# Optimization experiments

Measured on AMD Instinct MI355X. Metric: run time of the kernel, lower is better.

Reference implementation:

```python
import jax, jax.numpy as jnp
import numpy as np

T, D, H, S = 32768, 512, 1024, 256  # seq_len, observation_dim, hidden_size, state_dim


def setup_inputs() -> dict:
    key = jax.random.key(0)
    ks = jax.random.split(key, 8)
    lim_ih = 1.0 / np.sqrt(H)
    return {
        "y": jax.random.normal(ks[0], (T, D), dtype=jnp.float32),
        "h0": jax.random.normal(ks[1], (H,), dtype=jnp.float32),
        "w_ih": jax.random.uniform(ks[2], (3 * H, D), minval=-lim_ih, maxval=lim_ih, dtype=jnp.float32),
        "w_hh": jax.random.uniform(ks[3], (3 * H, H), minval=-lim_ih, maxval=lim_ih, dtype=jnp.float32),
        "b": jax.random.uniform(ks[4], (3 * H,), minval=-lim_ih, maxval=lim_ih, dtype=jnp.float32),
        "bn": jax.random.uniform(ks[5], (H,), minval=-lim_ih, maxval=lim_ih, dtype=jnp.float32),
        "w_out": jax.random.uniform(ks[6], (2 * S, H), minval=-lim_ih, maxval=lim_ih, dtype=jnp.float32),
        "b_out": jax.random.uniform(ks[7], (2 * S,), minval=-lim_ih, maxval=lim_ih, dtype=jnp.float32),
    }


def _gru_forward(y, h0, w_ih, w_hh, b, bn):
    # Precompute input-side gates for all timesteps in one GEMM: [T, 3H]
    igates = y @ w_ih.T + b

    def step(h, ig):
        ir, iz, inn = jnp.split(ig, 3)
        hg = w_hh @ h  # [3H]
        hr, hz, hn = jnp.split(hg, 3)
        r = jax.nn.sigmoid(ir + hr)
        z = jax.nn.sigmoid(iz + hz)  # equinox calls this `inp`
        n = jnp.tanh(inn + r * (hn + bn))
        h_new = n + z * (h - n)
        return h_new, h_new

    _, hs = jax.lax.scan(step, jnp.tanh(h0), igates)
    return hs  # [T, H]


def reference(y, h0, w_ih, w_hh, b, bn, w_out, b_out):
    hs = _gru_forward(y, h0, w_ih, w_hh, b, bn)
    out = hs @ w_out.T + b_out  # [T, 2S]
    nat1, nat2 = jnp.split(out, 2, axis=-1)
    return (nat1, jax.nn.softplus(nat2))
```

## Files before the change

### kernel.cpp

```cpp
#include <hip/hip_runtime.h>
#include <math.h>

#define T_STEPS 32768
#define DIM 512
#define HID 1024
#define SD 256

#define NWG 256
#define RBT 128

typedef unsigned u32x4 __attribute__((ext_vector_type(4)));

#define PIN4(v) asm volatile("" : "+v"((v).x), "+v"((v).y), "+v"((v).z), "+v"((v).w))

__device__ __forceinline__ float dot4(float4 a, float4 b) {
    return a.x*b.x + a.y*b.y + a.z*b.z + a.w*b.w;
}
__device__ __forceinline__ float sigmoid_fast(float x) {
    float e = __builtin_amdgcn_exp2f(-1.4426950408889634f * x);
    return __builtin_amdgcn_rcpf(1.f + e);
}
__device__ __forceinline__ float tanh_fast(float x) {
    float e = __builtin_amdgcn_exp2f(2.8853900817779268f * x);
    return 1.f - 2.f * __builtin_amdgcn_rcpf(e + 1.f);
}
__device__ __forceinline__ float softplus_f(float x) {
    float ax = fabsf(x);
    return fmaxf(x, 0.f) + log1pf(expf(-ax));
}
__device__ __forceinline__ float4 asf4(u32x4 q) {
    return make_float4(__uint_as_float(q.x), __uint_as_float(q.y),
                       __uint_as_float(q.z), __uint_as_float(q.w));
}

__device__ __forceinline__ float wave_sum(float v) {
    int x;
    x = __builtin_amdgcn_mov_dpp(__float_as_int(v), 0xB1,  0xf, 0xf, true); v += __int_as_float(x);
    x = __builtin_amdgcn_mov_dpp(__float_as_int(v), 0x4E,  0xf, 0xf, true); v += __int_as_float(x);
    x = __builtin_amdgcn_mov_dpp(__float_as_int(v), 0x141, 0xf, 0xf, true); v += __int_as_float(x);
    x = __builtin_amdgcn_mov_dpp(__float_as_int(v), 0x128, 0xf, 0xf, true); v += __int_as_float(x);
    v += __shfl_xor(v, 16, 64);
    v += __shfl_xor(v, 32, 64);
    return v;
}

__global__ void init_kernel(const float* __restrict__ h0,
                            unsigned* __restrict__ htag) {
    int i = blockIdx.x * 256 + threadIdx.x;
    unsigned v = __float_as_uint(tanhf(h0[i]));
    htag[i]       = v & ~3u;
    htag[HID + i] = 0u;
}

#define TAGCHK(m, tg)                                                          \
    m = ((q0.x ^ tg) | (q0.y ^ tg)) | ((q0.z ^ tg) | (q0.w ^ tg))              \
      | ((q1.x ^ tg) | (q1.y ^ tg)) | ((q1.z ^ tg) | (q1.w ^ tg))              \
      | ((q2.x ^ tg) | (q2.y ^ tg)) | ((q2.z ^ tg) | (q2.w ^ tg))              \
      | ((q3.x ^ tg) | (q3.y ^ tg)) | ((q3.z ^ tg) | (q3.w ^ tg))

__global__ __launch_bounds__(RBT, 1) void gru_scan(
    const float* __restrict__ y, const float* __restrict__ h0,
    const float* __restrict__ w_ih, const float* __restrict__ w_hh,
    const float* __restrict__ b, const float* __restrict__ bn,
    const float* __restrict__ w_out, const float* __restrict__ b_out,
    float* __restrict__ out, unsigned* __restrict__ htag ) {
    const int tid  = threadIdx.x;
    const int wg   = blockIdx.x;
    const int wv   = tid >> 6;
    const int lane = tid & 63;
    const int half = lane >> 5;
    const int u0   = wg * 4 + wv * 2;
    const int um   = u0 + half;

    float4 wh[3][2][4];
    #pragma unroll
    for (int g = 0; g < 3; ++g)
        #pragma unroll
        for (int uu = 0; uu < 2; ++uu) {
            const float* row = &w_hh[(size_t)(g * HID + u0 + uu) * HID + 16 * lane];
            #pragma unroll
            for (int q = 0; q < 4; ++q) { wh[g][uu][q] = *(const float4*)&row[4*q]; PIN4(wh[g][uu][q]); }
        }
    float4 wi[3][2][2];
    #pragma unroll
    for (int g = 0; g < 3; ++g)
        #pragma unroll
        for (int uu = 0; uu < 2; ++uu) {
            const float* row = &w_ih[(size_t)(g * HID + u0 + uu) * DIM + 8 * lane];
            #pragma unroll
            for (int q = 0; q < 2; ++q) { wi[g][uu][q] = *(const float4*)&row[4*q]; PIN4(wi[g][uu][q]); }
        }
    const int c = 2 * wg + wv;
    float4 wo[4];
    #pragma unroll
    for (int q = 0; q < 4; ++q) {
        wo[q] = *(const float4*)&w_out[(size_t)c * HID + 16 * lane + 4 * q];
        PIN4(wo[q]);
    }

    const float bi_r = b[um], bi_z = b[HID + um], bi_n = b[2 * HID + um];
    const float bnu  = bn[um];
    const float bo   = b_out[c];

    float hp = tanhf(h0[um]);

    float yr, yz, yi;
    {
        float4 ya0 = *(const float4*)&y[8 * lane];
        float4 ya1 = *(const float4*)&y[8 * lane + 4];
        float d[6];
        #pragma unroll
        for (int g = 0; g < 3; ++g)
            #pragma unroll
            for (int uu = 0; uu < 2; ++uu)
                d[g*2+uu] = dot4(wi[g][uu][0], ya0) + dot4(wi[g][uu][1], ya1);
        #pragma unroll
        for (int k = 0; k < 6; ++k) d[k] = wave_sum(d[k]);
        yr = (half ? d[1] : d[0]) + bi_r;
        yz = (half ? d[3] : d[2]) + bi_z;
        yi = (half ? d[5] : d[4]) + bi_n;
    }

    const size_t TS = (size_t)T_STEPS * SD;

    for (int t = 0; t <= T_STEPS; ++t) {
        const unsigned tg = (unsigned)t & 3u;
        const unsigned* pa = htag + (size_t)((t & 1) * HID + 16 * lane);
        const int tn = (t + 1 < T_STEPS) ? (t + 1) : 0;
        const float* ya = &y[(size_t)tn * DIM + 8 * lane];

        u32x4 q0, q1, q2, q3, yq0, yq1;
        asm volatile(
            "global_load_dwordx4 %[y0], %[ya], off\n\t"
            "global_load_dwordx4 %[y1], %[ya], off offset:16\n\t"
            "global_load_dwordx4 %[q0], %[pa], off sc0 sc1\n\t"
            "global_load_dwordx4 %[q1], %[pa], off offset:16 sc0 sc1\n\t"
            "global_load_dwordx4 %[q2], %[pa], off offset:32 sc0 sc1\n\t"
            "global_load_dwordx4 %[q3], %[pa], off offset:48 sc0 sc1\n\t"
            "s_waitcnt vmcnt(0)"
            : [q0]"=&v"(q0), [q1]"=&v"(q1), [q2]"=&v"(q2), [q3]"=&v"(q3),
              [y0]"=&v"(yq0), [y1]"=&v"(yq1)
            : [pa]"v"(pa), [ya]"v"(ya)
            : "memory");
        unsigned m; TAGCHK(m, tg);
        while ((m & 3u) != 0u) {
            asm volatile(
                "global_load_dwordx4 %[q0], %[pa], off sc0 sc1\n\t"
                "global_load_dwordx4 %[q1], %[pa], off offset:16 sc0 sc1\n\t"
                "global_load_dwordx4 %[q2], %[pa], off offset:32 sc0 sc1\n\t"
                "global_load_dwordx4 %[q3], %[pa], off offset:48 sc0 sc1\n\t"
                "s_waitcnt vmcnt(0)"
                : [q0]"=&v"(q0), [q1]"=&v"(q1), [q2]"=&v"(q2), [q3]"=&v"(q3)
                : [pa]"v"(pa)
                : "memory");
            TAGCHK(m, tg);
        }
        float4 hv0 = asf4(q0), hv1 = asf4(q1), hv2 = asf4(q2), hv3 = asf4(q3);

        if (t < T_STEPS) {
            float s[6];
            #pragma unroll
            for (int g = 0; g < 3; ++g)
                #pragma unroll
                for (int uu = 0; uu < 2; ++uu)
                    s[g*2+uu] = dot4(wh[g][uu][0], hv0) + dot4(wh[g][uu][1], hv1)
                              + dot4(wh[g][uu][2], hv2) + dot4(wh[g][uu][3], hv3);
            #pragma unroll
            for (int k = 0; k < 6; ++k) s[k] = wave_sum(s[k]);

            float r = sigmoid_fast((half ? s[1] : s[0]) + yr);
            float z = sigmoid_fast((half ? s[3] : s[2]) + yz);
            float n = tanh_fast(yi + r * ((half ? s[5] : s[4]) + bnu));
            float hnew = n + z * (hp - n);
            hp = hnew;

            if ((lane & 31) == 0) {
                unsigned pv = (__float_as_uint(hnew) & ~3u) | (((unsigned)t + 1u) & 3u);
                unsigned* pp = htag + (size_t)(((t + 1) & 1) * HID + um);
                asm volatile("global_store_dword %0, %1, off sc0 sc1"
                             :: "v"(pp), "v"(pv) : "memory");
            }
            __builtin_amdgcn_sched_barrier(0);
        }

        {
            float4 ya0 = asf4(yq0), ya1 = asf4(yq1);
            float d[6];
            #pragma unroll
            for (int g = 0; g < 3; ++g)
                #pragma unroll
                for (int uu = 0; uu < 2; ++uu)
                    d[g*2+uu] = dot4(wi[g][uu][0], ya0) + dot4(wi[g][uu][1], ya1);
            #pragma unroll
            for (int k = 0; k < 6; ++k) d[k] = wave_sum(d[k]);
            yr = (half ? d[1] : d[0]) + bi_r;
            yz = (half ? d[3] : d[2]) + bi_z;
            yi = (half ? d[5] : d[4]) + bi_n;
        }

        if (t > 0) {
            float p = dot4(wo[0], hv0) + dot4(wo[1], hv1)
                    + dot4(wo[2], hv2) + dot4(wo[3], hv3);
            p = wave_sum(p);
            if (lane == 0) {
                float v = p + bo;
                size_t row = (size_t)(t - 1);
                if (c >= SD) out[TS + row * SD + (c - SD)] = softplus_f(v);
                else         out[row * SD + c] = v;
            }
        }
    }
}

extern "C" void kernel_launch(void* const* d_in, const int* in_sizes, int n_in,
                              void* d_out, int out_size, void* d_ws, size_t ws_size,
                              hipStream_t stream) {
    const float* y     = (const float*)d_in[0];
    const float* h0    = (const float*)d_in[1];
    const float* w_ih  = (const float*)d_in[2];
    const float* w_hh  = (const float*)d_in[3];
    const float* b     = (const float*)d_in[4];
    const float* bn    = (const float*)d_in[5];
    const float* w_out = (const float*)d_in[6];
    const float* b_out = (const float*)d_in[7];
    float* out = (float*)d_out;

    unsigned* htag = (unsigned*)d_ws;

    hipLaunchKernelGGL(init_kernel, dim3(4), dim3(256), 0, stream, h0, htag);
    hipLaunchKernelGGL(gru_scan, dim3(NWG), dim3(RBT), 0, stream,
                       y, h0, w_ih, w_hh, b, bn, w_out, b_out, out, htag);
}
```

Before: 52.11 ms.

## Split GRU scan into recurrent and helper waves communicating through LDS

Doubles the workgroup to four waves: two waves handle only the recurrent w_hh matvec and global h exchange, while two helper waves compute the input projection for future timesteps and the output projection plus softplus. They hand off data through shared-memory ring buffers guarded by volatile sequence counters. The aim is to take the input-GEMV and output work off the serial critical path of each timestep. The cost is extra LDS traffic, intra-workgroup spin-waiting, and the risk that the helper waves fall behind and stall the recurrence.

```diff
diff --git a/kernel.cpp b/kernel.cpp
--- a/kernel.cpp
+++ b/kernel.cpp
@@ -7,7 +7,7 @@
 #define SD 256
 
 #define NWG 256
-#define RBT 128
+#define RBT 256
 
 typedef unsigned u32x4 __attribute__((ext_vector_type(4)));
 
@@ -52,11 +52,24 @@
     htag[HID + i] = 0u;
 }
 
-#define TAGCHK(m, tg)                                                          \
-    m = ((q0.x ^ tg) | (q0.y ^ tg)) | ((q0.z ^ tg) | (q0.w ^ tg))              \
-      | ((q1.x ^ tg) | (q1.y ^ tg)) | ((q1.z ^ tg) | (q1.w ^ tg))              \
-      | ((q2.x ^ tg) | (q2.y ^ tg)) | ((q2.z ^ tg) | (q2.w ^ tg))              \
-      | ((q3.x ^ tg) | (q3.y ^ tg)) | ((q3.z ^ tg) | (q3.w ^ tg))
+__device__ __forceinline__ void spin1(const unsigned* pa, unsigned tg,
+                                      u32x4& q0, u32x4& q1, u32x4& q2, u32x4& q3) {
+    for (;;) {
+        asm volatile(
+            "global_load_dwordx4 %0, %4, off sc0 sc1\n\t"
+            "global_load_dwordx4 %1, %4, off offset:16 sc0 sc1\n\t"
+            "global_load_dwordx4 %2, %4, off offset:32 sc0 sc1\n\t"
+            "global_load_dwordx4 %3, %4, off offset:48 sc0 sc1\n\t"
+            "s_waitcnt vmcnt(0)"
+            : "=&v"(q0), "=&v"(q1), "=&v"(q2), "=&v"(q3)
+            : "v"(pa) : "memory");
+        unsigned m = ((q0.x ^ tg) | (q0.y ^ tg)) | ((q0.z ^ tg) | (q0.w ^ tg))
+                   | ((q1.x ^ tg) | (q1.y ^ tg)) | ((q1.z ^ tg) | (q1.w ^ tg))
+                   | ((q2.x ^ tg) | (q2.y ^ tg)) | ((q2.z ^ tg) | (q2.w ^ tg))
+                   | ((q3.x ^ tg) | (q3.y ^ tg)) | ((q3.z ^ tg) | (q3.w ^ tg));
+        if ((m & 3u) == 0u) break;
+    }
+}
 
 __global__ __launch_bounds__(RBT, 1) void gru_scan(
     const float* __restrict__ y, const float* __restrict__ h0,
@@ -69,122 +82,120 @@
     const int wv   = tid >> 6;
     const int lane = tid & 63;
     const int half = lane >> 5;
-    const int u0   = wg * 4 + wv * 2;
-    const int um   = u0 + half;
-
-    float4 wh[3][2][4];
-    #pragma unroll
-    for (int g = 0; g < 3; ++g)
-        #pragma unroll
-        for (int uu = 0; uu < 2; ++uu) {
-            const float* row = &w_hh[(size_t)(g * HID + u0 + uu) * HID + 16 * lane];
-            #pragma unroll
-            for (int q = 0; q < 4; ++q) { wh[g][uu][q] = *(const float4*)&row[4*q]; PIN4(wh[g][uu][q]); }
+
+    __shared__ float hsh[2][HID];
+    __shared__ float ygv[4][2][6];
+    __shared__ int   seqH[2];
+    __shared__ int   seqY[8];
+    __shared__ int   prog[2];
+    if (tid < 2) { seqH[tid] = 0; prog[tid] = 0; }
+    if (tid < 8) seqY[tid] = 0;
+    __syncthreads();
+    volatile int* vseqH = seqH;
+    volatile int* vseqY = seqY;
+    volatile int* vprog = prog;
+
+    const size_t TS = (size_t)T_STEPS * SD;
+
+    if (wv < 2) {
+        const int u0 = wg * 4 + wv * 2;
+        const int um = u0 + half;
+
+        float4 wh[3][2][4];
+        #pragma unroll
+        for (int g = 0; g < 3; ++g)
+            #pragma unroll
+            for (int uu = 0; uu < 2; ++uu) {
+                const float* row = &w_hh[(size_t)(g * HID + u0 + uu) * HID + 16 * lane];
+                #pragma unroll
+                for (int q = 0; q < 4; ++q) { wh[g][uu][q] = *(const float4*)&row[4*q]; PIN4(wh[g][uu][q]); }
+            }
+        const float bnu = bn[um];
+        float hp = tanhf(h0[um]);
+
+        for (int t = 0; t <= T_STEPS; ++t) {
+            const unsigned tg = (unsigned)t & 3u;
+            const unsigned* pa = htag + (size_t)((t & 1) * HID + 16 * lane);
+            u32x4 q0, q1, q2, q3;
+            spin1(pa, tg, q0, q1, q2, q3);
+            float4 hv0 = asf4(q0), hv1 = asf4(q1), hv2 = asf4(q2), hv3 = asf4(q3);
+
+            if (t < T_STEPS) {
+                volatile int* sy = &vseqY[(t & 3) * 2 + wv];
+                while (*sy != t + 1) {}
+                asm volatile("" ::: "memory");
+                const float* yB = ygv[t & 3][wv];
+                float yr = yB[half * 3 + 0];
+                float yz = yB[half * 3 + 1];
+                float yi = yB[half * 3 + 2];
+
+                float s[6];
+                #pragma unroll
+                for (int g = 0; g < 3; ++g)
+                    #pragma unroll
+                    for (int uu = 0; uu < 2; ++uu)
+                        s[g*2+uu] = dot4(wh[g][uu][0], hv0) + dot4(wh[g][uu][1], hv1)
+                                  + dot4(wh[g][uu][2], hv2) + dot4(wh[g][uu][3], hv3);
+                #pragma unroll
+                for (int k = 0; k < 6; ++k) s[k] = wave_sum(s[k]);
+
+                float r = sigmoid_fast((half ? s[1] : s[0]) + yr);
+                float z = sigmoid_fast((half ? s[3] : s[2]) + yz);
+                float n = tanh_fast(yi + r * ((half ? s[5] : s[4]) + bnu));
+                float hnew = n + z * (hp - n);
+                hp = hnew;
+
+                if ((lane & 31) == 0) {
+                    unsigned pv = (__float_as_uint(hnew) & ~3u) | (((unsigned)t + 1u) & 3u);
+                    unsigned* pp = htag + (size_t)(((t + 1) & 1) * HID + um);
+                    asm volatile("global_store_dword %0, %1, off sc0 sc1"
+                                 :: "v"(pp), "v"(pv) : "memory");
+                }
+                __builtin_amdgcn_sched_barrier(0);
+            }
+
+            if (wv == 0) {
+                while (vprog[0] < t - 1 || vprog[1] < t - 1) {}
+                asm volatile("" ::: "memory");
+                float* hd = &hsh[t & 1][16 * lane];
+                *(float4*)&hd[0]  = hv0;
+                *(float4*)&hd[4]  = hv1;
+                *(float4*)&hd[8]  = hv2;
+                *(float4*)&hd[12] = hv3;
+                asm volatile("s_waitcnt lgkmcnt(0)" ::: "memory");
+                if (lane == 0) vseqH[t & 1] = t + 1;
+            }
         }
-    float4 wi[3][2][2];
-    #pragma unroll
-    for (int g = 0; g < 3; ++g)
-        #pragma unroll
-        for (int uu = 0; uu < 2; ++uu) {
-            const float* row = &w_ih[(size_t)(g * HID + u0 + uu) * DIM + 8 * lane];
-            #pragma unroll
-            for (int q = 0; q < 2; ++q) { wi[g][uu][q] = *(const float4*)&row[4*q]; PIN4(wi[g][uu][q]); }
+    } else {
+        const int hw  = wv - 2;
+        const int us0 = wg * 4 + hw * 2;
+
+        float4 wi[3][2][2];
+        #pragma unroll
+        for (int g = 0; g < 3; ++g)
+            #pragma unroll
+            for (int uu = 0; uu < 2; ++uu) {
+                const float* row = &w_ih[(size_t)(g * HID + us0 + uu) * DIM + 8 * lane];
+                #pragma unroll
+                for (int q = 0; q < 2; ++q) { wi[g][uu][q] = *(const float4*)&row[4*q]; PIN4(wi[g][uu][q]); }
+            }
+        const int c = 2 * wg + hw;
+        float4 wo[4];
+        #pragma unroll
+        for (int q = 0; q < 4; ++q) {
+            wo[q] = *(const float4*)&w_out[(size_t)c * HID + 16 * lane + 4 * q];
+            PIN4(wo[q]);
         }
-    const int c = 2 * wg + wv;
-    float4 wo[4];
-    #pragma unroll
-    for (int q = 0; q < 4; ++q) {
-        wo[q] = *(const float4*)&w_out[(size_t)c * HID + 16 * lane + 4 * q];
-        PIN4(wo[q]);
-    }
-
-    const float bi_r = b[um], bi_z = b[HID + um], bi_n = b[2 * HID + um];
-    const float bnu  = bn[um];
-    const float bo   = b_out[c];
-
-    float hp = tanhf(h0[um]);
-
-    float yr, yz, yi;
-    {
-        float4 ya0 = *(const float4*)&y[8 * lane];
-        float4 ya1 = *(const float4*)&y[8 * lane + 4];
-        float d[6];
+        const float bo = b_out[c];
+        float bb[6];
         #pragma unroll
         for (int g = 0; g < 3; ++g)
             #pragma unroll
-            for (int uu = 0; uu < 2; ++uu)
-                d[g*2+uu] = dot4(wi[g][uu][0], ya0) + dot4(wi[g][uu][1], ya1);
-        #pragma unroll
-        for (int k = 0; k < 6; ++k) d[k] = wave_sum(d[k]);
-        yr = (half ? d[1] : d[0]) + bi_r;
-        yz = (half ? d[3] : d[2]) + bi_z;
-        yi = (half ? d[5] : d[4]) + bi_n;
-    }
-
-    const size_t TS = (size_t)T_STEPS * SD;
-
-    for (int t = 0; t <= T_STEPS; ++t) {
-        const unsigned tg = (unsigned)t & 3u;
-        const unsigned* pa = htag + (size_t)((t & 1) * HID + 16 * lane);
-        const int tn = (t + 1 < T_STEPS) ? (t + 1) : 0;
-        const float* ya = &y[(size_t)tn * DIM + 8 * lane];
-
-        u32x4 q0, q1, q2, q3, yq0, yq1;
-        asm volatile(
-            "global_load_dwordx4 %[y0], %[ya], off\n\t"
-            "global_load_dwordx4 %[y1], %[ya], off offset:16\n\t"
-            "global_load_dwordx4 %[q0], %[pa], off sc0 sc1\n\t"
-            "global_load_dwordx4 %[q1], %[pa], off offset:16 sc0 sc1\n\t"
-            "global_load_dwordx4 %[q2], %[pa], off offset:32 sc0 sc1\n\t"
-            "global_load_dwordx4 %[q3], %[pa], off offset:48 sc0 sc1\n\t"
-            "s_waitcnt vmcnt(0)"
-            : [q0]"=&v"(q0), [q1]"=&v"(q1), [q2]"=&v"(q2), [q3]"=&v"(q3),
-              [y0]"=&v"(yq0), [y1]"=&v"(yq1)
-            : [pa]"v"(pa), [ya]"v"(ya)
-            : "memory");
-        unsigned m; TAGCHK(m, tg);
-        while ((m & 3u) != 0u) {
-            asm volatile(
-                "global_load_dwordx4 %[q0], %[pa], off sc0 sc1\n\t"
-                "global_load_dwordx4 %[q1], %[pa], off offset:16 sc0 sc1\n\t"
-                "global_load_dwordx4 %[q2], %[pa], off offset:32 sc0 sc1\n\t"
-                "global_load_dwordx4 %[q3], %[pa], off offset:48 sc0 sc1\n\t"
-                "s_waitcnt vmcnt(0)"
-                : [q0]"=&v"(q0), [q1]"=&v"(q1), [q2]"=&v"(q2), [q3]"=&v"(q3)
-                : [pa]"v"(pa)
-                : "memory");
-            TAGCHK(m, tg);
-        }
-        float4 hv0 = asf4(q0), hv1 = asf4(q1), hv2 = asf4(q2), hv3 = asf4(q3);
-
-        if (t < T_STEPS) {
-            float s[6];
-            #pragma unroll
-            for (int g = 0; g < 3; ++g)
-                #pragma unroll
-                for (int uu = 0; uu < 2; ++uu)
-                    s[g*2+uu] = dot4(wh[g][uu][0], hv0) + dot4(wh[g][uu][1], hv1)
-                              + dot4(wh[g][uu][2], hv2) + dot4(wh[g][uu][3], hv3);
-            #pragma unroll
-            for (int k = 0; k < 6; ++k) s[k] = wave_sum(s[k]);
-
-            float r = sigmoid_fast((half ? s[1] : s[0]) + yr);
-            float z = sigmoid_fast((half ? s[3] : s[2]) + yz);
-            float n = tanh_fast(yi + r * ((half ? s[5] : s[4]) + bnu));
-            float hnew = n + z * (hp - n);
-            hp = hnew;
-
-            if ((lane & 31) == 0) {
-                unsigned pv = (__float_as_uint(hnew) & ~3u) | (((unsigned)t + 1u) & 3u);
-                unsigned* pp = htag + (size_t)(((t + 1) & 1) * HID + um);
-                asm volatile("global_store_dword %0, %1, off sc0 sc1"
-                             :: "v"(pp), "v"(pv) : "memory");
-            }
-            __builtin_amdgcn_sched_barrier(0);
-        }
-
-        {
-            float4 ya0 = asf4(yq0), ya1 = asf4(yq1);
+            for (int uu = 0; uu < 2; ++uu) bb[g*2+uu] = b[g * HID + us0 + uu];
+
+        auto produceY = [&](int tp) {
+            float4 ya0 = *(const float4*)&y[(size_t)tp * DIM + 8 * lane];
+            float4 ya1 = *(const float4*)&y[(size_t)tp * DIM + 8 * lane + 4];
             float d[6];
             #pragma unroll
             for (int g = 0; g < 3; ++g)
@@ -192,24 +203,46 @@
                 for (int uu = 0; uu < 2; ++uu)
                     d[g*2+uu] = dot4(wi[g][uu][0], ya0) + dot4(wi[g][uu][1], ya1);
             #pragma unroll
-            for (int k = 0; k < 6; ++k) d[k] = wave_sum(d[k]);
-            yr = (half ? d[1] : d[0]) + bi_r;
-            yz = (half ? d[3] : d[2]) + bi_z;
-            yi = (half ? d[5] : d[4]) + bi_n;
-        }
-
-        if (t > 0) {
-            float p = dot4(wo[0], hv0) + dot4(wo[1], hv1)
-                    + dot4(wo[2], hv2) + dot4(wo[3], hv3);
-            p = wave_sum(p);
+            for (int k = 0; k < 6; ++k) d[k] = wave_sum(d[k]) + bb[k];
             if (lane == 0) {
-                float v = p + bo;
-                size_t row = (size_t)(t - 1);
-                if (c >= SD) out[TS + row * SD + (c - SD)] = softplus_f(v);
-                else         out[row * SD + c] = v;
-            }
+                float* e = ygv[tp & 3][hw];
+                e[0] = d[0]; e[1] = d[2]; e[2] = d[4];
+                e[3] = d[1]; e[4] = d[3]; e[5] = d[5];
+            }
+            asm volatile("s_waitcnt lgkmcnt(0)" ::: "memory");
+            if (lane == 0) vseqY[(tp & 3) * 2 + hw] = tp + 1;
+        };
+
+        produceY(0);
+        produceY(1);
+
+        for (int t = 0; t <= T_STEPS; ++t) {
+            volatile int* sh = &vseqH[t & 1];
+            while (*sh != t + 1) {}
+            asm volatile("" ::: "memory");
+            const float* hd = &hsh[t & 1][16 * lane];
+            float4 a0 = *(const float4*)&hd[0];
+            float4 a1 = *(const float4*)&hd[4];
+            float4 a2 = *(const float4*)&hd[8];
+            float4 a3 = *(const float4*)&hd[12];
+            asm volatile("s_waitcnt lgkmcnt(0)" ::: "memory");
+            if (lane == 0) vprog[hw] = t + 1;
+
+            if (t > 0) {
+                float p = dot4(wo[0], a0) + dot4(wo[1], a1)
+                        + dot4(wo[2], a2) + dot4(wo[3], a3);
+                p = wave_sum(p);
+                if (lane == 0) {
+                    float v = p + bo;
+                    size_t row = (size_t)(t - 1);
+                    if (c >= SD) out[TS + row * SD + (c - SD)] = softplus_f(v);
+                    else         out[row * SD + c] = v;
+                }
+            }
+            if (t + 2 < T_STEPS) produceY(t + 2);
         }
     }
+    asm volatile("s_waitcnt vmcnt(0)" ::: "memory");
 }
 
 extern "C" void kernel_launch(void* const* d_in, const int* in_sizes, int n_in,
```

Measured after the change: 150.3 ms. +188.5%, slower.

## Exchange hidden state as tagged bf16 pairs to halve per-step polling traffic

Applied to the files above, without the earlier changes.

The hidden state shared between workgroups each step is now packed as bf16 pairs, with a one-bit phase tag in each half-word's LSB, in place of fp32 words with 2-bit tags. Each lane polls 2 dwordx4 loads instead of 4, and one lane per wave writes a packed pair obtained via a cross-half shuffle. This shrinks the latency-bound global exchange on the sequential critical path. The cost is lower precision: h is rounded to bf16 with a truncated mantissa bit before the recurrent matvec and the output projection, which may hurt accuracy over 32768 steps.

```diff
diff --git a/kernel.cpp b/kernel.cpp
--- a/kernel.cpp
+++ b/kernel.cpp
@@ -28,9 +28,9 @@
     float ax = fabsf(x);
     return fmaxf(x, 0.f) + log1pf(expf(-ax));
 }
-__device__ __forceinline__ float4 asf4(u32x4 q) {
-    return make_float4(__uint_as_float(q.x), __uint_as_float(q.y),
-                       __uint_as_float(q.z), __uint_as_float(q.w));
+__device__ __forceinline__ unsigned bf16rne(float x) {
+    unsigned b = __float_as_uint(x);
+    return (b + 0x7FFFu + ((b >> 16) & 1u)) >> 16;
 }
 
 __device__ __forceinline__ float wave_sum(float v) {
@@ -45,25 +45,31 @@
 }
 
 __global__ void init_kernel(const float* __restrict__ h0,
-                            unsigned* __restrict__ htag) {
+                            unsigned* __restrict__ hb16) {
     int i = blockIdx.x * 256 + threadIdx.x;
-    unsigned v = __float_as_uint(tanhf(h0[i]));
-    htag[i]       = v & ~3u;
-    htag[HID + i] = 0u;
-}
-
-#define TAGCHK(m, tg)                                                          \
-    m = ((q0.x ^ tg) | (q0.y ^ tg)) | ((q0.z ^ tg) | (q0.w ^ tg))              \
-      | ((q1.x ^ tg) | (q1.y ^ tg)) | ((q1.z ^ tg) | (q1.w ^ tg))              \
-      | ((q2.x ^ tg) | (q2.y ^ tg)) | ((q2.z ^ tg) | (q2.w ^ tg))              \
-      | ((q3.x ^ tg) | (q3.y ^ tg)) | ((q3.z ^ tg) | (q3.w ^ tg))
+    if (i < 512) {
+        unsigned lo = bf16rne(tanhf(h0[2 * i]))     & 0xFFFEu;
+        unsigned hi = bf16rne(tanhf(h0[2 * i + 1])) & 0xFFFEu;
+        hb16[i] = lo | (hi << 16);
+    } else {
+        hb16[i] = 0x00010001u;
+    }
+}
+
+#define TAGM(m, pat)                                                           \
+    m = ((q0.x ^ pat) | (q0.y ^ pat)) | ((q0.z ^ pat) | (q0.w ^ pat))          \
+      | ((q1.x ^ pat) | (q1.y ^ pat)) | ((q1.z ^ pat) | (q1.w ^ pat))
+
+#define UNPK(w, lo, hi)                                                        \
+    lo = __uint_as_float((w << 16) & 0xFFFE0000u);                             \
+    hi = __uint_as_float(w & 0xFFFE0000u);
 
 __global__ __launch_bounds__(RBT, 1) void gru_scan(
     const float* __restrict__ y, const float* __restrict__ h0,
     const float* __restrict__ w_ih, const float* __restrict__ w_hh,
     const float* __restrict__ b, const float* __restrict__ bn,
     const float* __restrict__ w_out, const float* __restrict__ b_out,
-    float* __restrict__ out, unsigned* __restrict__ htag ) {
+    float* __restrict__ out, unsigned* __restrict__ hb16 ) {
     const int tid  = threadIdx.x;
     const int wg   = blockIdx.x;
     const int wv   = tid >> 6;
@@ -124,38 +130,37 @@
     const size_t TS = (size_t)T_STEPS * SD;
 
     for (int t = 0; t <= T_STEPS; ++t) {
-        const unsigned tg = (unsigned)t & 3u;
-        const unsigned* pa = htag + (size_t)((t & 1) * HID + 16 * lane);
+        const unsigned pat = (((unsigned)t >> 1) & 1u) * 0x00010001u;
+        const unsigned* pa = hb16 + (size_t)((t & 1) * 512 + 8 * lane);
         const int tn = (t + 1 < T_STEPS) ? (t + 1) : 0;
         const float* ya = &y[(size_t)tn * DIM + 8 * lane];
 
-        u32x4 q0, q1, q2, q3, yq0, yq1;
+        u32x4 q0, q1, yq0, yq1;
         asm volatile(
             "global_load_dwordx4 %[y0], %[ya], off\n\t"
             "global_load_dwordx4 %[y1], %[ya], off offset:16\n\t"
             "global_load_dwordx4 %[q0], %[pa], off sc0 sc1\n\t"
             "global_load_dwordx4 %[q1], %[pa], off offset:16 sc0 sc1\n\t"
-            "global_load_dwordx4 %[q2], %[pa], off offset:32 sc0 sc1\n\t"
-            "global_load_dwordx4 %[q3], %[pa], off offset:48 sc0 sc1\n\t"
             "s_waitcnt vmcnt(0)"
-            : [q0]"=&v"(q0), [q1]"=&v"(q1), [q2]"=&v"(q2), [q3]"=&v"(q3),
-              [y0]"=&v"(yq0), [y1]"=&v"(yq1)
+            : [q0]"=&v"(q0), [q1]"=&v"(q1), [y0]"=&v"(yq0), [y1]"=&v"(yq1)
             : [pa]"v"(pa), [ya]"v"(ya)
             : "memory");
-        unsigned m; TAGCHK(m, tg);
-        while ((m & 3u) != 0u) {
+        unsigned m; TAGM(m, pat);
+        while ((m & 0x00010001u) != 0u) {
             asm volatile(
                 "global_load_dwordx4 %[q0], %[pa], off sc0 sc1\n\t"
                 "global_load_dwordx4 %[q1], %[pa], off offset:16 sc0 sc1\n\t"
-                "global_load_dwordx4 %[q2], %[pa], off offset:32 sc0 sc1\n\t"
-                "global_load_dwordx4 %[q3], %[pa], off offset:48 sc0 sc1\n\t"
                 "s_waitcnt vmcnt(0)"
-                : [q0]"=&v"(q0), [q1]"=&v"(q1), [q2]"=&v"(q2), [q3]"=&v"(q3)
+                : [q0]"=&v"(q0), [q1]"=&v"(q1)
                 : [pa]"v"(pa)
                 : "memory");
-            TAGCHK(m, tg);
-        }
-        float4 hv0 = asf4(q0), hv1 = asf4(q1), hv2 = asf4(q2), hv3 = asf4(q3);
+            TAGM(m, pat);
+        }
+        float4 hv0, hv1, hv2, hv3;
+        UNPK(q0.x, hv0.x, hv0.y) UNPK(q0.y, hv0.z, hv0.w)
+        UNPK(q0.z, hv1.x, hv1.y) UNPK(q0.w, hv1.z, hv1.w)
+        UNPK(q1.x, hv2.x, hv2.y) UNPK(q1.y, hv2.z, hv2.w)
+        UNPK(q1.z, hv3.x, hv3.y) UNPK(q1.w, hv3.z, hv3.w)
 
         if (t < T_STEPS) {
             float s[6];
@@ -174,9 +179,12 @@
             float hnew = n + z * (hp - n);
             hp = hnew;
 
-            if ((lane & 31) == 0) {
-                unsigned pv = (__float_as_uint(hnew) & ~3u) | (((unsigned)t + 1u) & 3u);
-                unsigned* pp = htag + (size_t)(((t + 1) & 1) * HID + um);
+            unsigned u16 = bf16rne(hnew) & 0xFFFEu;
+            unsigned other = __shfl_xor(u16, 32, 64);
+            if (lane == 0) {
+                unsigned tb1 = (((unsigned)t + 1u) >> 1) & 1u;
+                unsigned pv = (u16 | tb1) | ((other | tb1) << 16);
+                unsigned* pp = hb16 + (size_t)(((t + 1) & 1) * 512 + (2 * wg + wv));
                 asm volatile("global_store_dword %0, %1, off sc0 sc1"
                              :: "v"(pp), "v"(pv) : "memory");
             }
@@ -184,7 +192,10 @@
         }
 
         {
-            float4 ya0 = asf4(yq0), ya1 = asf4(yq1);
+            float4 ya0 = make_float4(__uint_as_float(yq0.x), __uint_as_float(yq0.y),
+                                     __uint_as_float(yq0.z), __uint_as_float(yq0.w));
+            float4 ya1 = make_float4(__uint_as_float(yq1.x), __uint_as_float(yq1.y),
+                                     __uint_as_float(yq1.z), __uint_as_float(yq1.w));
             float d[6];
             #pragma unroll
             for (int g = 0; g < 3; ++g)
@@ -210,6 +221,7 @@
             }
         }
     }
+    asm volatile("s_waitcnt vmcnt(0)" ::: "memory");
 }
 
 extern "C" void kernel_launch(void* const* d_in, const int* in_sizes, int n_in,
@@ -225,9 +237,9 @@
     const float* b_out = (const float*)d_in[7];
     float* out = (float*)d_out;
 
-    unsigned* htag = (unsigned*)d_ws;
-
-    hipLaunchKernelGGL(init_kernel, dim3(4), dim3(256), 0, stream, h0, htag);
+    unsigned* hb16 = (unsigned*)d_ws;
+
+    hipLaunchKernelGGL(init_kernel, dim3(4), dim3(256), 0, stream, h0, hb16);
     hipLaunchKernelGGL(gru_scan, dim3(NWG), dim3(RBT), 0, stream,
-                       y, h0, w_ih, w_hh, b, bn, w_out, b_out, out, htag);
-}
+                       y, h0, w_ih, w_hh, b, bn, w_out, b_out, out, hb16);
+}
```

Result: slower. 60.93 ms (+16.9%).
